# Kernel tuning notes

Hardware: AMD Instinct MI355X
Metric: run time of the kernel (lower is better)

Reference implementation:

```python
import jax, jax.numpy as jnp
import numpy as np

L, D, H, DH, S, B, V = 8, 1024, 16, 64, 1024, 4, 32000
EPS = 1e-5


def layernorm(x, s, b):
    m = x.mean(-1, keepdims=True)
    v = ((x - m) ** 2).mean(-1, keepdims=True)
    return (x - m) * jax.lax.rsqrt(v + EPS) * s + b


def setup_inputs() -> dict:
    key = jax.random.key(0)
    ks = jax.random.split(key, 12)
    sd = 0.02
    inp = {
        'idx': jax.random.randint(ks[0], (B, S), 0, V),
        'tok_emb': jax.random.normal(ks[1], (V, D), jnp.float32) * sd,
        'pos_emb': jax.random.normal(ks[2], (S, D), jnp.float32) * sd,
        'ln1_s': jnp.ones((L, D), jnp.float32),
        'ln1_b': jnp.zeros((L, D), jnp.float32),
        'wq': jax.random.normal(ks[3], (L, H, D, DH), jnp.float32) * sd,
        'wk': jax.random.normal(ks[4], (L, H, D, DH), jnp.float32) * sd,
        'wv': jax.random.normal(ks[5], (L, H, D, DH), jnp.float32) * sd,
        'wproj': jax.random.normal(ks[6], (L, D, D), jnp.float32) * sd,  # stored [D_in, D_out]
        'ln2_s': jnp.ones((L, D), jnp.float32),
        'ln2_b': jnp.zeros((L, D), jnp.float32),
        'w1': jax.random.normal(ks[7], (L, D, 4 * D), jnp.float32) * sd,
        'b1': jnp.zeros((L, 4 * D), jnp.float32),
        'w2': jax.random.normal(ks[8], (L, 4 * D, D), jnp.float32) * sd,
        'b2': jnp.zeros((L, D), jnp.float32),
        'lnf_s': jnp.ones((D,), jnp.float32),
        'lnf_b': jnp.zeros((D,), jnp.float32),
        'lm_w': jax.random.normal(ks[9], (D, V), jnp.float32) * sd,  # stored [D_in, V]
        'lm_b': jnp.zeros((V,), jnp.float32),
    }
    return inp


def reference(idx, tok_emb, pos_emb, ln1_s, ln1_b, wq, wk, wv, wproj,
              ln2_s, ln2_b, w1, b1, w2, b2, lnf_s, lnf_b, lm_w, lm_b):
    T = idx.shape[1]
    x = tok_emb[idx] + pos_emb[:T]  # [B,T,D]
    mask = jnp.tril(jnp.ones((T, T), bool))
    scale = DH ** -0.5
    for l in range(L):  # fixed small layer count
        h = layernorm(x, ln1_s[l], ln1_b[l])
        q = jnp.einsum('bsd,hde->bhse', h, wq[l])
        k = jnp.einsum('bsd,hde->bhse', h, wk[l])
        v = jnp.einsum('bsd,hde->bhse', h, wv[l])
        att = jnp.einsum('bhse,bhte->bhst', q, k) * scale
        att = jnp.where(mask, att, -jnp.inf)
        att = jax.nn.softmax(att, axis=-1)  # dropout=0.0 -> identity
        o = jnp.einsum('bhst,bhte->bhse', att, v)
        o = o.transpose(0, 2, 1, 3).reshape(x.shape)  # concat heads: [B,T,H*DH]
        x = x + o @ wproj[l]
        h2 = layernorm(x, ln2_s[l], ln2_b[l])
        x = x + jax.nn.relu(h2 @ w1[l] + b1[l]) @ w2[l] + b2[l]
    x = layernorm(x, lnf_s, lnf_b)
    logits = x @ lm_w + lm_b  # [B,T,V]
    return logits
```

## Files before the change

kernel.cpp:

```cpp
#include <hip/hip_runtime.h>
#include <hip/hip_bf16.h>

#define LL 8
#define DD 1024
#define HH 16
#define DHH 64
#define SS 1024
#define BB 4
#define VV 32000
#define MM (BB * SS)

typedef unsigned short u16;
typedef __attribute__((ext_vector_type(8))) short short8v;
typedef __attribute__((ext_vector_type(4))) float f32x4;
typedef unsigned int __attribute__((address_space(1))) guint;
typedef unsigned int __attribute__((address_space(3))) luint;

__device__ __forceinline__ float bf2f_lo(unsigned u) { return __uint_as_float(u << 16); }
__device__ __forceinline__ u16 f2bf(float f) {
  unsigned x = __float_as_uint(f);
  return (u16)((x + 0x7fffu + ((x >> 16) & 1u)) >> 16);
}

__global__ __launch_bounds__(256) void embed_kernel(
    const int* __restrict__ idx, const float* __restrict__ tok,
    const float* __restrict__ pos, float* __restrict__ x) {
  int i = blockIdx.x * blockDim.x + threadIdx.x;
  int elem = i * 4;
  int row = elem / DD;
  int d = elem % DD;
  int s = row % SS;
  int t = idx[row];
  float4 tv = *(const float4*)(tok + (size_t)t * DD + d);
  float4 pv = *(const float4*)(pos + (size_t)s * DD + d);
  tv.x += pv.x; tv.y += pv.y; tv.z += pv.z; tv.w += pv.w;
  *(float4*)(x + (size_t)elem) = tv;
}

__global__ __launch_bounds__(256) void ln_bf16_kernel(
    const float* __restrict__ x, const float* __restrict__ sc,
    const float* __restrict__ bi, u16* __restrict__ out) {
  const int row = blockIdx.x;
  const int tid = threadIdx.x;
  __shared__ float red[4];
  float4 v = ((const float4*)(x + (size_t)row * DD))[tid];
  float s = v.x + v.y + v.z + v.w;
  #pragma unroll
  for (int off = 32; off; off >>= 1) s += __shfl_down(s, off);
  if ((tid & 63) == 0) red[tid >> 6] = s;
  __syncthreads();
  float mean = (red[0] + red[1] + red[2] + red[3]) * (1.f / DD);
  float dx = v.x - mean, dy = v.y - mean, dz = v.z - mean, dw = v.w - mean;
  float vs = dx * dx + dy * dy + dz * dz + dw * dw;
  __syncthreads();
  #pragma unroll
  for (int off = 32; off; off >>= 1) vs += __shfl_down(vs, off);
  if ((tid & 63) == 0) red[tid >> 6] = vs;
  __syncthreads();
  float var = (red[0] + red[1] + red[2] + red[3]) * (1.f / DD);
  float rstd = rsqrtf(var + 1e-5f);
  float4 s4 = ((const float4*)sc)[tid];
  float4 b4 = ((const float4*)bi)[tid];
  ushort4 o;
  o.x = f2bf(dx * rstd * s4.x + b4.x);
  o.y = f2bf(dy * rstd * s4.y + b4.y);
  o.z = f2bf(dz * rstd * s4.z + b4.z);
  o.w = f2bf(dw * rstd * s4.w + b4.w);
  *(ushort4*)(out + (size_t)row * DD + tid * 4) = o;
}

template <bool HEADW>
__global__ __launch_bounds__(256) void convT_kernel(
    const float* __restrict__ W, u16* __restrict__ BT, int K, int N,
    size_t lstride) {
  __shared__ float tile[32][33];
  const int n0 = blockIdx.x * 32, k0 = blockIdx.y * 32, l = blockIdx.z;
  const int tx = threadIdx.x & 31, ty = threadIdx.x >> 5;
  const float* Wl;
  int ld;
  if (HEADW) {
    const int h = n0 >> 6;
    Wl = W + ((size_t)(l * HH + h) * K) * 64 + (n0 & 63);
    ld = 64;
  } else {
    Wl = W + (size_t)l * K * N + n0;
    ld = N;
  }
  #pragma unroll
  for (int i = 0; i < 4; ++i)
    tile[ty + 8 * i][tx] = Wl[(size_t)(k0 + ty + 8 * i) * ld + tx];
  __syncthreads();
  u16* out = BT + (size_t)l * lstride;
  #pragma unroll
  for (int i = 0; i < 4; ++i)
    out[(size_t)(n0 + ty + 8 * i) * K + k0 + tx] = f2bf(tile[tx][ty + 8 * i]);
}

__global__ __launch_bounds__(256) void transpose_v(
    const u16* __restrict__ qkv, u16* __restrict__ vt) {
  __shared__ u16 t[32][33];
  const int s0 = blockIdx.x * 32, d0 = blockIdx.y * 32;
  const int tx = threadIdx.x & 31, ty = threadIdx.x >> 5;
  #pragma unroll
  for (int i = 0; i < 4; ++i)
    t[ty + 8 * i][tx] = qkv[(size_t)(s0 + ty + 8 * i) * 3072 + 2048 + d0 + tx];
  __syncthreads();
  #pragma unroll
  for (int i = 0; i < 4; ++i)
    vt[(size_t)(d0 + ty + 8 * i) * MM + s0 + tx] = t[tx][ty + 8 * i];
}

#define BARRIER __builtin_amdgcn_s_barrier()
#define MEMFENCE asm volatile("" ::: "memory")

#define LDA_(BUF, KH, F) \
  (*(const short8v*)&As[BUF][KH][(wm * 128 + (F) * 16 + (lane & 15)) * 32 + rg])
#define LDB_(BUF, KH, NF) \
  (*(const short8v*)&Bs[BUF][KH][(wn * 64 + (NF) * 16 + (lane & 15)) * 32 + rg])
#define LDS_A(S0,S1,S2,S3, BUF, KH, FB) { \
  S0 = LDA_(BUF, KH, (FB) + 0); S1 = LDA_(BUF, KH, (FB) + 1); \
  S2 = LDA_(BUF, KH, (FB) + 2); S3 = LDA_(BUF, KH, (FB) + 3); }
#define LDS_B(S0,S1,S2,S3, BUF, KH) { \
  S0 = LDB_(BUF, KH, 0); S1 = LDB_(BUF, KH, 1); \
  S2 = LDB_(BUF, KH, 2); S3 = LDB_(BUF, KH, 3); }
#define STAGE_A(BUF, KH, KT) do { \
  __builtin_amdgcn_global_load_lds((const guint*)(Abase + (KT) * 64 + (KH) * 32), \
      (luint*)(&As[BUF][KH][tid * 8]), 16, 0, 0); \
  __builtin_amdgcn_global_load_lds((const guint*)(Abase + (size_t)128 * K + (KT) * 64 + (KH) * 32), \
      (luint*)(&As[BUF][KH][(tid + 512) * 8]), 16, 0, 0); \
} while (0)
#define STAGE_B(BUF, KH, KT) do { \
  __builtin_amdgcn_global_load_lds((const guint*)(Bbase + (KT) * 64 + (KH) * 32), \
      (luint*)(&Bs[BUF][KH][tid * 8]), 16, 0, 0); \
  __builtin_amdgcn_global_load_lds((const guint*)(Bbase + (size_t)128 * K + (KT) * 64 + (KH) * 32), \
      (luint*)(&Bs[BUF][KH][(tid + 512) * 8]), 16, 0, 0); \
} while (0)
#define MROW(F, AQ, B0,B1,B2,B3) \
  acc[F][0] = __builtin_amdgcn_mfma_f32_16x16x32_bf16(AQ, B0, acc[F][0], 0, 0, 0); \
  acc[F][1] = __builtin_amdgcn_mfma_f32_16x16x32_bf16(AQ, B1, acc[F][1], 0, 0, 0); \
  acc[F][2] = __builtin_amdgcn_mfma_f32_16x16x32_bf16(AQ, B2, acc[F][2], 0, 0, 0); \
  acc[F][3] = __builtin_amdgcn_mfma_f32_16x16x32_bf16(AQ, B3, acc[F][3], 0, 0, 0);
#define MFMA16S(FB, A0,A1,A2,A3, B0,B1,B2,B3) \
  MROW((FB) + 0, A0, B0,B1,B2,B3) MROW((FB) + 1, A1, B0,B1,B2,B3) \
  MROW((FB) + 2, A2, B0,B1,B2,B3) MROW((FB) + 3, A3, B0,B1,B2,B3)

#define TILE4(CUR, KT, ST1, ST2, V1STR, V3STR, LD4, LGK4STR) { \
  const int cur_ = (CUR); \
   \
  MEMFENCE; \
  LDS_A(aN0,aN1,aN2,aN3, cur_, 0, 4); \
  if (ST1) { STAGE_A(cur_ ^ 1, 1, (KT) + 1); } \
  asm volatile("s_waitcnt " V1STR ::: "memory"); \
  asm volatile("s_waitcnt lgkmcnt(4)" ::: "memory"); \
  BARRIER; \
  __builtin_amdgcn_s_setprio(1); \
  MFMA16S(0, aP0,aP1,aP2,aP3, bP0,bP1,bP2,bP3); \
  __builtin_amdgcn_s_setprio(0); \
   \
  MEMFENCE; \
  LDS_A(aP0,aP1,aP2,aP3, cur_, 1, 0); \
  LDS_B(bN0,bN1,bN2,bN3, cur_, 1); \
  if (ST1) { STAGE_B(cur_ ^ 1, 1, (KT) + 1); } \
  asm volatile("s_waitcnt lgkmcnt(8)" ::: "memory"); \
  BARRIER; \
  __builtin_amdgcn_s_setprio(1); \
  MFMA16S(4, aN0,aN1,aN2,aN3, bP0,bP1,bP2,bP3); \
  __builtin_amdgcn_s_setprio(0); \
   \
  MEMFENCE; \
  LDS_A(aN0,aN1,aN2,aN3, cur_, 1, 4); \
  if (ST2) { STAGE_A(cur_, 0, (KT) + 2); } \
  asm volatile("s_waitcnt " V3STR ::: "memory"); \
  asm volatile("s_waitcnt lgkmcnt(4)" ::: "memory"); \
  BARRIER; \
  __builtin_amdgcn_s_setprio(1); \
  MFMA16S(0, aP0,aP1,aP2,aP3, bN0,bN1,bN2,bN3); \
  __builtin_amdgcn_s_setprio(0); \
   \
  MEMFENCE; \
  if (LD4) { LDS_A(aP0,aP1,aP2,aP3, cur_ ^ 1, 0, 0); \
             LDS_B(bP0,bP1,bP2,bP3, cur_ ^ 1, 0); } \
  if (ST2) { STAGE_B(cur_, 0, (KT) + 2); } \
  asm volatile("s_waitcnt " LGK4STR ::: "memory"); \
  BARRIER; \
  __builtin_amdgcn_s_setprio(1); \
  MFMA16S(4, aN0,aN1,aN2,aN3, bN0,bN1,bN2,bN3); \
  __builtin_amdgcn_s_setprio(0); \
}

template <bool BIAS, bool RELU, bool RESID, bool OBF16>
__global__ __launch_bounds__(512, 2) void gemm8(
    const u16* __restrict__ A, const u16* __restrict__ BT,
    const float* __restrict__ bias, const float* __restrict__ resid,
    void* __restrict__ Cv, int M, int N, int K) {
  __shared__ u16 As[2][2][8192];
  __shared__ u16 Bs[2][2][8192];
  const int tid = threadIdx.x;
  const int lane = tid & 63, wave = tid >> 6;
  const int wm = wave >> 2, wn = wave & 3;
  const int nwg = gridDim.x;
  const int bid = blockIdx.x;
  const int wg = ((nwg & 7) == 0) ? ((bid & 7) * (nwg >> 3) + (bid >> 3)) : bid;
  const int nmt = M >> 8;
  const int m0 = (wg % nmt) * 256;
  const int n0 = (wg / nmt) * 256;
  const int NT = K >> 6;
  const int sr = tid >> 2;
  const int ssc = (((tid & 3) ^ ((tid >> 3) & 3)) * 8);
  const u16* Abase = A + (size_t)(m0 + sr) * K + ssc;
  const u16* Bbase = BT + (size_t)(n0 + sr) * K + ssc;
  const int rg = (((lane >> 4) ^ ((lane >> 1) & 3)) * 8);

  f32x4 acc[8][4] = {};
  short8v aP0, aP1, aP2, aP3, aN0, aN1, aN2, aN3;
  short8v bP0, bP1, bP2, bP3, bN0, bN1, bN2, bN3;

  STAGE_A(0, 0, 0); STAGE_B(0, 0, 0);
  STAGE_A(0, 1, 0); STAGE_B(0, 1, 0);
  STAGE_A(1, 0, 1); STAGE_B(1, 0, 1);
  asm volatile("s_waitcnt vmcnt(8)" ::: "memory");
  BARRIER;
  MEMFENCE;
  LDS_A(aP0,aP1,aP2,aP3, 0, 0, 0);
  LDS_B(bP0,bP1,bP2,bP3, 0, 0);

  int kt = 0;
  for (; kt < NT - 2; ++kt) {
    TILE4(kt & 1, kt, true, true, "vmcnt(6)", "vmcnt(6)", true, "lgkmcnt(8)");
  }
  TILE4(kt & 1, kt, true, false, "vmcnt(6)", "vmcnt(4)", true, "lgkmcnt(8)");
  ++kt;
  TILE4(kt & 1, kt, false, false, "vmcnt(0)", "vmcnt(0)", false, "lgkmcnt(0)");

  #pragma unroll
  for (int f = 0; f < 8; ++f) {
    #pragma unroll
    for (int n = 0; n < 4; ++n) {
      const int col = n0 + wn * 64 + n * 16 + (lane & 15);
      #pragma unroll
      for (int r = 0; r < 4; ++r) {
        const int row = m0 + wm * 128 + f * 16 + (lane >> 4) * 4 + r;
        float v = acc[f][n][r];
        if (BIAS) v += bias[col];
        if (RELU) v = fmaxf(v, 0.f);
        if (RESID) v += resid[(size_t)row * N + col];
        if (OBF16)
          ((u16*)Cv)[(size_t)row * N + col] = f2bf(v);
        else
          ((float*)Cv)[(size_t)row * N + col] = v;
      }
    }
  }
}

#define LDA4_(BUF, KH, F) \
  (*(const short8v*)&As[BUF][KH][(wm * 64 + (F) * 16 + (lane & 15)) * 32 + rg])
#define LDB4_(BUF, KH, NF) \
  (*(const short8v*)&Bs[BUF][KH][(wn * 64 + (NF) * 16 + (lane & 15)) * 32 + rg])
#define STAGE_A4(BUF, KH, KT) do { \
  __builtin_amdgcn_global_load_lds((const guint*)(Abase + (KT) * 64 + (KH) * 32), \
      (luint*)(&As[BUF][KH][tid * 8]), 16, 0, 0); \
  __builtin_amdgcn_global_load_lds((const guint*)(Abase + (size_t)64 * K + (KT) * 64 + (KH) * 32), \
      (luint*)(&As[BUF][KH][(tid + 256) * 8]), 16, 0, 0); \
} while (0)
#define STAGE_B4(BUF, KH, KT) do { \
  __builtin_amdgcn_global_load_lds((const guint*)(Bbase + (KT) * 64 + (KH) * 32), \
      (luint*)(&Bs[BUF][KH][tid * 8]), 16, 0, 0); \
  __builtin_amdgcn_global_load_lds((const guint*)(Bbase + (size_t)64 * K + (KT) * 64 + (KH) * 32), \
      (luint*)(&Bs[BUF][KH][(tid + 256) * 8]), 16, 0, 0); \
} while (0)
#define MFMA8S(F0, F1, A0, A1, B0,B1,B2,B3) \
  MROW(F0, A0, B0,B1,B2,B3) MROW(F1, A1, B0,B1,B2,B3)

#define TILE4P(CUR, KT, ST1, ST2, V1STR, V3STR, LD4, LGK4STR) { \
  const int cur_ = (CUR); \
   \
  MEMFENCE; \
  aN0 = LDA4_(cur_, 0, 2); aN1 = LDA4_(cur_, 0, 3); \
  if (ST1) { STAGE_A4(cur_ ^ 1, 1, (KT) + 1); } \
  asm volatile("s_waitcnt " V1STR ::: "memory"); \
  asm volatile("s_waitcnt lgkmcnt(2)" ::: "memory"); \
  BARRIER; \
  __builtin_amdgcn_s_setprio(1); \
  MFMA8S(0, 1, aP0, aP1, bP0,bP1,bP2,bP3); \
  __builtin_amdgcn_s_setprio(0); \
   \
  MEMFENCE; \
  aP0 = LDA4_(cur_, 1, 0); aP1 = LDA4_(cur_, 1, 1); \
  bN0 = LDB4_(cur_, 1, 0); bN1 = LDB4_(cur_, 1, 1); \
  bN2 = LDB4_(cur_, 1, 2); bN3 = LDB4_(cur_, 1, 3); \
  if (ST1) { STAGE_B4(cur_ ^ 1, 1, (KT) + 1); } \
  asm volatile("s_waitcnt lgkmcnt(6)" ::: "memory"); \
  BARRIER; \
  __builtin_amdgcn_s_setprio(1); \
  MFMA8S(2, 3, aN0, aN1, bP0,bP1,bP2,bP3); \
  __builtin_amdgcn_s_setprio(0); \
   \
  MEMFENCE; \
  aN0 = LDA4_(cur_, 1, 2); aN1 = LDA4_(cur_, 1, 3); \
  if (ST2) { STAGE_A4(cur_, 0, (KT) + 2); } \
  asm volatile("s_waitcnt " V3STR ::: "memory"); \
  asm volatile("s_waitcnt lgkmcnt(2)" ::: "memory"); \
  BARRIER; \
  __builtin_amdgcn_s_setprio(1); \
  MFMA8S(0, 1, aP0, aP1, bN0,bN1,bN2,bN3); \
  __builtin_amdgcn_s_setprio(0); \
   \
  MEMFENCE; \
  if (LD4) { aP0 = LDA4_(cur_ ^ 1, 0, 0); aP1 = LDA4_(cur_ ^ 1, 0, 1); \
             bP0 = LDB4_(cur_ ^ 1, 0, 0); bP1 = LDB4_(cur_ ^ 1, 0, 1); \
             bP2 = LDB4_(cur_ ^ 1, 0, 2); bP3 = LDB4_(cur_ ^ 1, 0, 3); } \
  if (ST2) { STAGE_B4(cur_, 0, (KT) + 2); } \
  asm volatile("s_waitcnt " LGK4STR ::: "memory"); \
  BARRIER; \
  __builtin_amdgcn_s_setprio(1); \
  MFMA8S(2, 3, aN0, aN1, bN0,bN1,bN2,bN3); \
  __builtin_amdgcn_s_setprio(0); \
}

template <bool BIAS, bool RELU, bool RESID, bool OBF16>
__global__ __launch_bounds__(256, 2) void gemm4p(
    const u16* __restrict__ A, const u16* __restrict__ BT,
    const float* __restrict__ bias, const float* __restrict__ resid,
    void* __restrict__ Cv, int M, int N, int K) {
  __shared__ u16 As[2][2][4096];
  __shared__ u16 Bs[2][2][4096];
  const int tid = threadIdx.x;
  const int lane = tid & 63, wave = tid >> 6;
  const int wm = wave >> 1, wn = wave & 1;
  const int m0 = blockIdx.x * 128, n0 = blockIdx.y * 128;
  const int NT = K >> 6;
  const int sr = tid >> 2;
  const int ssc = (((tid & 3) ^ ((tid >> 3) & 3)) * 8);
  const u16* Abase = A + (size_t)(m0 + sr) * K + ssc;
  const u16* Bbase = BT + (size_t)(n0 + sr) * K + ssc;
  const int rg = (((lane >> 4) ^ ((lane >> 1) & 3)) * 8);

  f32x4 acc[4][4] = {};
  short8v aP0, aP1, aN0, aN1;
  short8v bP0, bP1, bP2, bP3, bN0, bN1, bN2, bN3;

  STAGE_A4(0, 0, 0); STAGE_B4(0, 0, 0);
  STAGE_A4(0, 1, 0); STAGE_B4(0, 1, 0);
  STAGE_A4(1, 0, 1); STAGE_B4(1, 0, 1);
  asm volatile("s_waitcnt vmcnt(8)" ::: "memory");
  BARRIER;
  MEMFENCE;
  aP0 = LDA4_(0, 0, 0); aP1 = LDA4_(0, 0, 1);
  bP0 = LDB4_(0, 0, 0); bP1 = LDB4_(0, 0, 1);
  bP2 = LDB4_(0, 0, 2); bP3 = LDB4_(0, 0, 3);

  int kt = 0;
  for (; kt < NT - 2; ++kt) {
    TILE4P(kt & 1, kt, true, true, "vmcnt(6)", "vmcnt(6)", true, "lgkmcnt(6)");
  }
  TILE4P(kt & 1, kt, true, false, "vmcnt(6)", "vmcnt(4)", true, "lgkmcnt(6)");
  ++kt;
  TILE4P(kt & 1, kt, false, false, "vmcnt(0)", "vmcnt(0)", false, "lgkmcnt(0)");

  #pragma unroll
  for (int f = 0; f < 4; ++f) {
    #pragma unroll
    for (int n = 0; n < 4; ++n) {
      const int col = n0 + wn * 64 + n * 16 + (lane & 15);
      #pragma unroll
      for (int r = 0; r < 4; ++r) {
        const int row = m0 + wm * 64 + f * 16 + (lane >> 4) * 4 + r;
        float v = acc[f][n][r];
        if (BIAS) v += bias[col];
        if (RELU) v = fmaxf(v, 0.f);
        if (RESID) v += resid[(size_t)row * N + col];
        if (OBF16)
          ((u16*)Cv)[(size_t)row * N + col] = f2bf(v);
        else
          ((float*)Cv)[(size_t)row * N + col] = v;
      }
    }
  }
}

__global__ __launch_bounds__(256) void gemm_fb(
    const u16* __restrict__ A, const float* __restrict__ B,
    const float* __restrict__ bias, float* __restrict__ C, int M, int N, int K) {
  __shared__ alignas(16) float Asm[16][68];
  __shared__ alignas(16) float Bsm[16][68];
  const int tid = threadIdx.x;
  const int tx = tid & 15, ty = tid >> 4;
  const int m0 = blockIdx.y * 64, n0 = blockIdx.x * 64;
  const int ar = tid >> 2, ac = (tid & 3) * 4;
  const int br = tid >> 4, bc = (tid & 15) * 4;
  float acc[4][4] = {};
  for (int k0 = 0; k0 < K; k0 += 16) {
    ushort4 au = *(const ushort4*)(A + (size_t)(m0 + ar) * K + k0 + ac);
    float4 bv = *(const float4*)(B + (size_t)(k0 + br) * N + n0 + bc);
    Asm[ac + 0][ar] = bf2f_lo(au.x);
    Asm[ac + 1][ar] = bf2f_lo(au.y);
    Asm[ac + 2][ar] = bf2f_lo(au.z);
    Asm[ac + 3][ar] = bf2f_lo(au.w);
    *(float4*)&Bsm[br][bc] = bv;
    __syncthreads();
    #pragma unroll
    for (int kk = 0; kk < 16; ++kk) {
      float4 a = *(const float4*)&Asm[kk][ty * 4];
      float4 b = *(const float4*)&Bsm[kk][tx * 4];
      acc[0][0] += a.x * b.x; acc[0][1] += a.x * b.y; acc[0][2] += a.x * b.z; acc[0][3] += a.x * b.w;
      acc[1][0] += a.y * b.x; acc[1][1] += a.y * b.y; acc[1][2] += a.y * b.z; acc[1][3] += a.y * b.w;
      acc[2][0] += a.z * b.x; acc[2][1] += a.z * b.y; acc[2][2] += a.z * b.z; acc[2][3] += a.z * b.w;
      acc[3][0] += a.w * b.x; acc[3][1] += a.w * b.y; acc[3][2] += a.w * b.z; acc[3][3] += a.w * b.w;
    }
    __syncthreads();
  }
  #pragma unroll
  for (int i = 0; i < 4; ++i) {
    const int m = m0 + ty * 4 + i;
    #pragma unroll
    for (int j = 0; j < 4; ++j) {
      const int n = n0 + tx * 4 + j;
      C[(size_t)m * N + n] = acc[i][j] + bias[n];
    }
  }
}

__global__ __launch_bounds__(256) void attn_mfma(
    const u16* __restrict__ qkv, const u16* __restrict__ vt,
    u16* __restrict__ o) {
  __shared__ alignas(16) u16 Ksh[64 * 64];
  __shared__ alignas(16) u16 Vsh[64 * 64];
  __shared__ unsigned Plds[4][16 * 41];
  __shared__ float bcast[4][16];
  const int tid = threadIdx.x;
  const int lane = tid & 63, wave = tid >> 6;
  const int g = lane >> 4, qi = lane & 15;
  const int qt = blockIdx.x, h = blockIdx.y, b = blockIdx.z;
  const int q0w = qt * 64 + wave * 16;
  const int qloc = wave * 16 + qi;

  short8v qf0, qf1;
  {
    const u16* qp = qkv + ((size_t)b * SS + q0w + qi) * 3072 + h * DHH + g * 8;
    qf0 = *(const short8v*)qp;
    qf1 = *(const short8v*)(qp + 32);
  }

  f32x4 oacc[4] = {};
  float mrow = -1e30f, lrow = 0.f;

  for (int kt = 0; kt <= qt; ++kt) {
    __syncthreads();
    #pragma unroll
    for (int u = 0; u < 2; ++u) {
      const int unit = tid + 256 * u;
      const int row = unit >> 3, ch = unit & 7;
      const int sch = ch ^ (row & 7);
      __builtin_amdgcn_global_load_lds(
          (const guint*)(qkv + ((size_t)b * SS + kt * 64 + row) * 3072 + 1024 + h * DHH + sch * 8),
          (luint*)(Ksh + unit * 8), 16, 0, 0);
      __builtin_amdgcn_global_load_lds(
          (const guint*)(vt + ((size_t)(h * DHH + row)) * MM + b * SS + kt * 64 + sch * 8),
          (luint*)(Vsh + unit * 8), 16, 0, 0);
    }
    __syncthreads();

    f32x4 st[4] = {};
    #pragma unroll
    for (int t = 0; t < 4; ++t) {
      const int row = t * 16 + qi;
      const int swz = (row & 7) << 4;
      short8v kf0 = *(const short8v*)(Ksh + row * 64 + (((g * 16) ^ swz) >> 1));
      short8v kf1 = *(const short8v*)(Ksh + row * 64 + (((64 + g * 16) ^ swz) >> 1));
      st[t] = __builtin_amdgcn_mfma_f32_16x16x32_bf16(kf0, qf0, st[t], 0, 0, 0);
      st[t] = __builtin_amdgcn_mfma_f32_16x16x32_bf16(kf1, qf1, st[t], 0, 0, 0);
    }

    if (kt == qt) {
      #pragma unroll
      for (int t = 0; t < 4; ++t)
        #pragma unroll
        for (int r = 0; r < 4; ++r)
          if (t * 16 + 4 * g + r > qloc) st[t][r] = -1e30f;
    }

    float mt = st[0][0];
    #pragma unroll
    for (int t = 0; t < 4; ++t)
      #pragma unroll
      for (int r = 0; r < 4; ++r) mt = fmaxf(mt, st[t][r]);
    mt = fmaxf(mt, __shfl_xor(mt, 16));
    mt = fmaxf(mt, __shfl_xor(mt, 32));
    const float mnew = fmaxf(mrow, mt * 0.125f);
    const float corr = __expf(mrow - mnew);
    float pl = 0.f;
    #pragma unroll
    for (int t = 0; t < 4; ++t) {
      #pragma unroll
      for (int r2 = 0; r2 < 2; ++r2) {
        float plo = __expf(fmaf(st[t][2 * r2], 0.125f, -mnew));
        float phi = __expf(fmaf(st[t][2 * r2 + 1], 0.125f, -mnew));
        pl += plo + phi;
        Plds[wave][qi * 41 + 8 * t + 2 * g + r2] =
            (unsigned)f2bf(plo) | ((unsigned)f2bf(phi) << 16);
      }
    }
    pl += __shfl_xor(pl, 16);
    pl += __shfl_xor(pl, 32);
    lrow = lrow * corr + pl;
    mrow = mnew;

    if (g == 0) bcast[wave][qi] = corr;
    float c0 = bcast[wave][g * 4 + 0];
    float c1 = bcast[wave][g * 4 + 1];
    float c2 = bcast[wave][g * 4 + 2];
    float c3 = bcast[wave][g * 4 + 3];
    #pragma unroll
    for (int dvt = 0; dvt < 4; ++dvt) {
      oacc[dvt][0] *= c0; oacc[dvt][1] *= c1;
      oacc[dvt][2] *= c2; oacc[dvt][3] *= c3;
    }

    union U8 { unsigned u[4]; short8v s8; };
    U8 pa0, pa1;
    #pragma unroll
    for (int c = 0; c < 4; ++c) {
      pa0.u[c] = Plds[wave][qi * 41 + g * 4 + c];
      pa1.u[c] = Plds[wave][qi * 41 + 16 + g * 4 + c];
    }
    #pragma unroll
    for (int dvt = 0; dvt < 4; ++dvt) {
      const int row = dvt * 16 + qi;
      const int swz = (row & 7) << 4;
      short8v v0 = *(const short8v*)(Vsh + row * 64 + (((g * 16) ^ swz) >> 1));
      short8v v1 = *(const short8v*)(Vsh + row * 64 + (((64 + g * 16) ^ swz) >> 1));
      oacc[dvt] = __builtin_amdgcn_mfma_f32_16x16x32_bf16(pa0.s8, v0, oacc[dvt], 0, 0, 0);
      oacc[dvt] = __builtin_amdgcn_mfma_f32_16x16x32_bf16(pa1.s8, v1, oacc[dvt], 0, 0, 0);
    }
  }

  if (g == 0) bcast[wave][qi] = 1.f / lrow;
  float i0 = bcast[wave][g * 4 + 0];
  float i1 = bcast[wave][g * 4 + 1];
  float i2 = bcast[wave][g * 4 + 2];
  float i3 = bcast[wave][g * 4 + 3];
  #pragma unroll
  for (int dvt = 0; dvt < 4; ++dvt) {
    const int col = h * DHH + dvt * 16 + qi;
    o[((size_t)b * SS + q0w + g * 4 + 0) * DD + col] = f2bf(oacc[dvt][0] * i0);
    o[((size_t)b * SS + q0w + g * 4 + 1) * DD + col] = f2bf(oacc[dvt][1] * i1);
    o[((size_t)b * SS + q0w + g * 4 + 2) * DD + col] = f2bf(oacc[dvt][2] * i2);
    o[((size_t)b * SS + q0w + g * 4 + 3) * DD + col] = f2bf(oacc[dvt][3] * i3);
  }
}

extern "C" void kernel_launch(void* const* d_in, const int* in_sizes, int n_in,
                              void* d_out, int out_size, void* d_ws, size_t ws_size,
                              hipStream_t stream) {
  const int* idx = (const int*)d_in[0];
  const float* tok_emb = (const float*)d_in[1];
  const float* pos_emb = (const float*)d_in[2];
  const float* ln1_s = (const float*)d_in[3];
  const float* ln1_b = (const float*)d_in[4];
  const float* wq = (const float*)d_in[5];
  const float* wk = (const float*)d_in[6];
  const float* wv = (const float*)d_in[7];
  const float* wproj = (const float*)d_in[8];
  const float* ln2_s = (const float*)d_in[9];
  const float* ln2_b = (const float*)d_in[10];
  const float* w1 = (const float*)d_in[11];
  const float* b1 = (const float*)d_in[12];
  const float* w2 = (const float*)d_in[13];
  const float* b2 = (const float*)d_in[14];
  const float* lnf_s = (const float*)d_in[15];
  const float* lnf_b = (const float*)d_in[16];
  const float* lm_w = (const float*)d_in[17];
  const float* lm_b = (const float*)d_in[18];

  const size_t MD = (size_t)MM * DD;

  u16* sc0 = (u16*)d_out;
  u16* BTqkv = sc0;
  u16* BTp = BTqkv + (size_t)LL * 3072 * DD;
  u16* BTw1 = BTp + (size_t)LL * DD * DD;
  u16* BTw2 = BTw1 + (size_t)LL * DD * 4 * DD;
  u16* qkvb = BTw2 + (size_t)LL * DD * 4 * DD;
  u16* vtb = qkvb + (size_t)MM * 3072;
  u16* ob = vtb + MD;
  u16* tmp = ob + MD;

  float* x = (float*)d_ws;
  u16* h = (u16*)((char*)d_ws + MD * 4);
  u16* BTlm = (u16*)((char*)d_ws + MD * 4 + MD * 2);
  const bool big_ws = ws_size >= (MD * 4 + MD * 2 + (size_t)VV * DD * 2);

  const dim3 blk(256);

  convT_kernel<true><<<dim3(DD / 32, DD / 32, LL), blk, 0, stream>>>(
      wq, BTqkv, DD, DD, (size_t)3072 * DD);
  convT_kernel<true><<<dim3(DD / 32, DD / 32, LL), blk, 0, stream>>>(
      wk, BTqkv + (size_t)DD * DD, DD, DD, (size_t)3072 * DD);
  convT_kernel<true><<<dim3(DD / 32, DD / 32, LL), blk, 0, stream>>>(
      wv, BTqkv + (size_t)2 * DD * DD, DD, DD, (size_t)3072 * DD);
  convT_kernel<false><<<dim3(DD / 32, DD / 32, LL), blk, 0, stream>>>(
      wproj, BTp, DD, DD, (size_t)DD * DD);
  convT_kernel<false><<<dim3(4 * DD / 32, DD / 32, LL), blk, 0, stream>>>(
      w1, BTw1, DD, 4 * DD, (size_t)DD * 4 * DD);
  convT_kernel<false><<<dim3(DD / 32, 4 * DD / 32, LL), blk, 0, stream>>>(
      w2, BTw2, 4 * DD, DD, (size_t)4 * DD * DD);
  if (big_ws)
    convT_kernel<false><<<dim3(VV / 32, DD / 32, 1), blk, 0, stream>>>(
        lm_w, BTlm, DD, VV, (size_t)VV * DD);

  embed_kernel<<<(MM * DD / 4 + 255) / 256, blk, 0, stream>>>(idx, tok_emb, pos_emb, x);

  for (int l = 0; l < LL; ++l) {
    ln_bf16_kernel<<<MM, blk, 0, stream>>>(x, ln1_s + l * DD, ln1_b + l * DD, h);
    gemm8<false, false, false, true><<<dim3((MM / 256) * (3072 / 256)), dim3(512), 0, stream>>>(
        h, BTqkv + (size_t)l * 3072 * DD, nullptr, nullptr, qkvb, MM, 3072, DD);
    transpose_v<<<dim3(MM / 32, DD / 32), blk, 0, stream>>>(qkvb, vtb);
    attn_mfma<<<dim3(SS / 64, HH, BB), blk, 0, stream>>>(qkvb, vtb, ob);
    gemm4p<false, false, true, false><<<dim3(MM / 128, DD / 128), blk, 0, stream>>>(
        ob, BTp + (size_t)l * DD * DD, nullptr, x, x, MM, DD, DD);
    ln_bf16_kernel<<<MM, blk, 0, stream>>>(x, ln2_s + l * DD, ln2_b + l * DD, h);
    gemm8<true, true, false, true><<<dim3((MM / 256) * (4 * DD / 256)), dim3(512), 0, stream>>>(
        h, BTw1 + (size_t)l * DD * 4 * DD, b1 + (size_t)l * 4 * DD, nullptr, tmp,
        MM, 4 * DD, DD);
    gemm4p<true, false, true, false><<<dim3(MM / 128, DD / 128), blk, 0, stream>>>(
        tmp, BTw2 + (size_t)l * 4 * DD * DD, b2 + (size_t)l * DD, x, x, MM, DD, 4 * DD);
  }

  ln_bf16_kernel<<<MM, blk, 0, stream>>>(x, lnf_s, lnf_b, h);
  if (big_ws) {
    gemm8<true, false, false, false><<<dim3((MM / 256) * (VV / 256)), dim3(512), 0, stream>>>(
        h, BTlm, lm_b, nullptr, (float*)d_out, MM, VV, DD);
  } else {
    gemm_fb<<<dim3(VV / 64, MM / 64), blk, 0, stream>>>(
        h, lm_w, lm_b, (float*)d_out, MM, VV, DD);
  }
}
```

Measured before the change: 2.429 ms.

## Enlarge attention query tile to 128 rows with 8 waves and reverse block order

The attention kernel now runs 512 threads (8 waves) per block, covering 128 query rows instead of 64. Each K/V tile loaded into shared memory is therefore reused by twice as many waves, halving global K/V traffic per query. Block indices are reversed so the longest causal blocks are scheduled first for better load balance. Waves whose queries lie entirely before the current key tile skip compute but still join the barriers, which leaves some MFMA work idle and halves the grid size.

Measured after the change: 2.392 ms. No clear change (-1.5%).

```diff
diff --git a/kernel.cpp b/kernel.cpp
--- a/kernel.cpp
+++ b/kernel.cpp
@@ -112,6 +112,11 @@
 
 #define BARRIER __builtin_amdgcn_s_barrier()
 #define MEMFENCE asm volatile("" ::: "memory")
+#define MROW(F, AQ, B0,B1,B2,B3) \
+  acc[F][0] = __builtin_amdgcn_mfma_f32_16x16x32_bf16(AQ, B0, acc[F][0], 0, 0, 0); \
+  acc[F][1] = __builtin_amdgcn_mfma_f32_16x16x32_bf16(AQ, B1, acc[F][1], 0, 0, 0); \
+  acc[F][2] = __builtin_amdgcn_mfma_f32_16x16x32_bf16(AQ, B2, acc[F][2], 0, 0, 0); \
+  acc[F][3] = __builtin_amdgcn_mfma_f32_16x16x32_bf16(AQ, B3, acc[F][3], 0, 0, 0);
 
 #define LDA_(BUF, KH, F) \
   (*(const short8v*)&As[BUF][KH][(wm * 128 + (F) * 16 + (lane & 15)) * 32 + rg])
@@ -135,11 +140,6 @@
   __builtin_amdgcn_global_load_lds((const guint*)(Bbase + (size_t)128 * K + (KT) * 64 + (KH) * 32), \
       (luint*)(&Bs[BUF][KH][(tid + 512) * 8]), 16, 0, 0); \
 } while (0)
-#define MROW(F, AQ, B0,B1,B2,B3) \
-  acc[F][0] = __builtin_amdgcn_mfma_f32_16x16x32_bf16(AQ, B0, acc[F][0], 0, 0, 0); \
-  acc[F][1] = __builtin_amdgcn_mfma_f32_16x16x32_bf16(AQ, B1, acc[F][1], 0, 0, 0); \
-  acc[F][2] = __builtin_amdgcn_mfma_f32_16x16x32_bf16(AQ, B2, acc[F][2], 0, 0, 0); \
-  acc[F][3] = __builtin_amdgcn_mfma_f32_16x16x32_bf16(AQ, B3, acc[F][3], 0, 0, 0);
 #define MFMA16S(FB, A0,A1,A2,A3, B0,B1,B2,B3) \
   MROW((FB) + 0, A0, B0,B1,B2,B3) MROW((FB) + 1, A1, B0,B1,B2,B3) \
   MROW((FB) + 2, A2, B0,B1,B2,B3) MROW((FB) + 3, A3, B0,B1,B2,B3)
@@ -274,7 +274,6 @@
 
 #define TILE4P(CUR, KT, ST1, ST2, V1STR, V3STR, LD4, LGK4STR) { \
   const int cur_ = (CUR); \
-   \
   MEMFENCE; \
   aN0 = LDA4_(cur_, 0, 2); aN1 = LDA4_(cur_, 0, 3); \
   if (ST1) { STAGE_A4(cur_ ^ 1, 1, (KT) + 1); } \
@@ -284,7 +283,6 @@
   __builtin_amdgcn_s_setprio(1); \
   MFMA8S(0, 1, aP0, aP1, bP0,bP1,bP2,bP3); \
   __builtin_amdgcn_s_setprio(0); \
-   \
   MEMFENCE; \
   aP0 = LDA4_(cur_, 1, 0); aP1 = LDA4_(cur_, 1, 1); \
   bN0 = LDB4_(cur_, 1, 0); bN1 = LDB4_(cur_, 1, 1); \
@@ -295,7 +293,6 @@
   __builtin_amdgcn_s_setprio(1); \
   MFMA8S(2, 3, aN0, aN1, bP0,bP1,bP2,bP3); \
   __builtin_amdgcn_s_setprio(0); \
-   \
   MEMFENCE; \
   aN0 = LDA4_(cur_, 1, 2); aN1 = LDA4_(cur_, 1, 3); \
   if (ST2) { STAGE_A4(cur_, 0, (KT) + 2); } \
@@ -305,7 +302,6 @@
   __builtin_amdgcn_s_setprio(1); \
   MFMA8S(0, 1, aP0, aP1, bN0,bN1,bN2,bN3); \
   __builtin_amdgcn_s_setprio(0); \
-   \
   MEMFENCE; \
   if (LD4) { aP0 = LDA4_(cur_ ^ 1, 0, 0); aP1 = LDA4_(cur_ ^ 1, 0, 1); \
              bP0 = LDB4_(cur_ ^ 1, 0, 0); bP1 = LDB4_(cur_ ^ 1, 0, 1); \
@@ -421,19 +417,20 @@
   }
 }
 
-__global__ __launch_bounds__(256) void attn_mfma(
+__global__ __launch_bounds__(512) void attn_mfma(
     const u16* __restrict__ qkv, const u16* __restrict__ vt,
     u16* __restrict__ o) {
   __shared__ alignas(16) u16 Ksh[64 * 64];
   __shared__ alignas(16) u16 Vsh[64 * 64];
-  __shared__ unsigned Plds[4][16 * 41];
-  __shared__ float bcast[4][16];
+  __shared__ unsigned Plds[8][16 * 41];
+  __shared__ float bcast[8][16];
   const int tid = threadIdx.x;
   const int lane = tid & 63, wave = tid >> 6;
   const int g = lane >> 4, qi = lane & 15;
-  const int qt = blockIdx.x, h = blockIdx.y, b = blockIdx.z;
-  const int q0w = qt * 64 + wave * 16;
-  const int qloc = wave * 16 + qi;
+  const int qt = (SS / 128 - 1) - blockIdx.x;
+  const int h = blockIdx.y, b = blockIdx.z;
+  const int q0w = qt * 128 + wave * 16;
+  const int ktmax = 2 * qt + 1;
 
   short8v qf0, qf1;
   {
@@ -445,93 +442,95 @@
   f32x4 oacc[4] = {};
   float mrow = -1e30f, lrow = 0.f;
 
-  for (int kt = 0; kt <= qt; ++kt) {
+  for (int kt = 0; kt <= ktmax; ++kt) {
     __syncthreads();
-    #pragma unroll
-    for (int u = 0; u < 2; ++u) {
-      const int unit = tid + 256 * u;
-      const int row = unit >> 3, ch = unit & 7;
+    {
+      const int row = tid >> 3, ch = tid & 7;
       const int sch = ch ^ (row & 7);
       __builtin_amdgcn_global_load_lds(
           (const guint*)(qkv + ((size_t)b * SS + kt * 64 + row) * 3072 + 1024 + h * DHH + sch * 8),
-          (luint*)(Ksh + unit * 8), 16, 0, 0);
+          (luint*)(Ksh + tid * 8), 16, 0, 0);
       __builtin_amdgcn_global_load_lds(
           (const guint*)(vt + ((size_t)(h * DHH + row)) * MM + b * SS + kt * 64 + sch * 8),
-          (luint*)(Vsh + unit * 8), 16, 0, 0);
+          (luint*)(Vsh + tid * 8), 16, 0, 0);
     }
     __syncthreads();
 
-    f32x4 st[4] = {};
-    #pragma unroll
-    for (int t = 0; t < 4; ++t) {
-      const int row = t * 16 + qi;
-      const int swz = (row & 7) << 4;
-      short8v kf0 = *(const short8v*)(Ksh + row * 64 + (((g * 16) ^ swz) >> 1));
-      short8v kf1 = *(const short8v*)(Ksh + row * 64 + (((64 + g * 16) ^ swz) >> 1));
-      st[t] = __builtin_amdgcn_mfma_f32_16x16x32_bf16(kf0, qf0, st[t], 0, 0, 0);
-      st[t] = __builtin_amdgcn_mfma_f32_16x16x32_bf16(kf1, qf1, st[t], 0, 0, 0);
-    }
-
-    if (kt == qt) {
+    const bool active = (kt * 64 <= q0w + 15);
+    if (active) {
+      f32x4 st[4] = {};
+      #pragma unroll
+      for (int t = 0; t < 4; ++t) {
+        const int row = t * 16 + qi;
+        const int swz = (row & 7) << 4;
+        short8v kf0 = *(const short8v*)(Ksh + row * 64 + (((g * 16) ^ swz) >> 1));
+        short8v kf1 = *(const short8v*)(Ksh + row * 64 + (((64 + g * 16) ^ swz) >> 1));
+        st[t] = __builtin_amdgcn_mfma_f32_16x16x32_bf16(kf0, qf0, st[t], 0, 0, 0);
+        st[t] = __builtin_amdgcn_mfma_f32_16x16x32_bf16(kf1, qf1, st[t], 0, 0, 0);
+      }
+
+      const int diag = q0w + qi - kt * 64;
+      if (diag < 63) {
+        #pragma unroll
+        for (int t = 0; t < 4; ++t)
+          #pragma unroll
+          for (int r = 0; r < 4; ++r)
+            if (t * 16 + 4 * g + r > diag) st[t][r] = -1e30f;
+      }
+
+      float mt = st[0][0];
       #pragma unroll
       for (int t = 0; t < 4; ++t)
         #pragma unroll
-        for (int r = 0; r < 4; ++r)
-          if (t * 16 + 4 * g + r > qloc) st[t][r] = -1e30f;
-    }
-
-    float mt = st[0][0];
-    #pragma unroll
-    for (int t = 0; t < 4; ++t)
-      #pragma unroll
-      for (int r = 0; r < 4; ++r) mt = fmaxf(mt, st[t][r]);
-    mt = fmaxf(mt, __shfl_xor(mt, 16));
-    mt = fmaxf(mt, __shfl_xor(mt, 32));
-    const float mnew = fmaxf(mrow, mt * 0.125f);
-    const float corr = __expf(mrow - mnew);
-    float pl = 0.f;
-    #pragma unroll
-    for (int t = 0; t < 4; ++t) {
-      #pragma unroll
-      for (int r2 = 0; r2 < 2; ++r2) {
-        float plo = __expf(fmaf(st[t][2 * r2], 0.125f, -mnew));
-        float phi = __expf(fmaf(st[t][2 * r2 + 1], 0.125f, -mnew));
-        pl += plo + phi;
-        Plds[wave][qi * 41 + 8 * t + 2 * g + r2] =
-            (unsigned)f2bf(plo) | ((unsigned)f2bf(phi) << 16);
-      }
-    }
-    pl += __shfl_xor(pl, 16);
-    pl += __shfl_xor(pl, 32);
-    lrow = lrow * corr + pl;
-    mrow = mnew;
-
-    if (g == 0) bcast[wave][qi] = corr;
-    float c0 = bcast[wave][g * 4 + 0];
-    float c1 = bcast[wave][g * 4 + 1];
-    float c2 = bcast[wave][g * 4 + 2];
-    float c3 = bcast[wave][g * 4 + 3];
-    #pragma unroll
-    for (int dvt = 0; dvt < 4; ++dvt) {
-      oacc[dvt][0] *= c0; oacc[dvt][1] *= c1;
-      oacc[dvt][2] *= c2; oacc[dvt][3] *= c3;
-    }
-
-    union U8 { unsigned u[4]; short8v s8; };
-    U8 pa0, pa1;
-    #pragma unroll
-    for (int c = 0; c < 4; ++c) {
-      pa0.u[c] = Plds[wave][qi * 41 + g * 4 + c];
-      pa1.u[c] = Plds[wave][qi * 41 + 16 + g * 4 + c];
-    }
-    #pragma unroll
-    for (int dvt = 0; dvt < 4; ++dvt) {
-      const int row = dvt * 16 + qi;
-      const int swz = (row & 7) << 4;
-      short8v v0 = *(const short8v*)(Vsh + row * 64 + (((g * 16) ^ swz) >> 1));
-      short8v v1 = *(const short8v*)(Vsh + row * 64 + (((64 + g * 16) ^ swz) >> 1));
-      oacc[dvt] = __builtin_amdgcn_mfma_f32_16x16x32_bf16(pa0.s8, v0, oacc[dvt], 0, 0, 0);
-      oacc[dvt] = __builtin_amdgcn_mfma_f32_16x16x32_bf16(pa1.s8, v1, oacc[dvt], 0, 0, 0);
+        for (int r = 0; r < 4; ++r) mt = fmaxf(mt, st[t][r]);
+      mt = fmaxf(mt, __shfl_xor(mt, 16));
+      mt = fmaxf(mt, __shfl_xor(mt, 32));
+      const float mnew = fmaxf(mrow, mt * 0.125f);
+      const float corr = __expf(mrow - mnew);
+      float pl = 0.f;
+      #pragma unroll
+      for (int t = 0; t < 4; ++t) {
+        #pragma unroll
+        for (int r2 = 0; r2 < 2; ++r2) {
+          float plo = __expf(fmaf(st[t][2 * r2], 0.125f, -mnew));
+          float phi = __expf(fmaf(st[t][2 * r2 + 1], 0.125f, -mnew));
+          pl += plo + phi;
+          Plds[wave][qi * 41 + 8 * t + 2 * g + r2] =
+              (unsigned)f2bf(plo) | ((unsigned)f2bf(phi) << 16);
+        }
+      }
+      pl += __shfl_xor(pl, 16);
+      pl += __shfl_xor(pl, 32);
+      lrow = lrow * corr + pl;
+      mrow = mnew;
+
+      if (g == 0) bcast[wave][qi] = corr;
+      float c0 = bcast[wave][g * 4 + 0];
+      float c1 = bcast[wave][g * 4 + 1];
+      float c2 = bcast[wave][g * 4 + 2];
+      float c3 = bcast[wave][g * 4 + 3];
+      #pragma unroll
+      for (int dvt = 0; dvt < 4; ++dvt) {
+        oacc[dvt][0] *= c0; oacc[dvt][1] *= c1;
+        oacc[dvt][2] *= c2; oacc[dvt][3] *= c3;
+      }
+
+      union U8 { unsigned u[4]; short8v s8; };
+      U8 pa0, pa1;
+      #pragma unroll
+      for (int c = 0; c < 4; ++c) {
+        pa0.u[c] = Plds[wave][qi * 41 + g * 4 + c];
+        pa1.u[c] = Plds[wave][qi * 41 + 16 + g * 4 + c];
+      }
+      #pragma unroll
+      for (int dvt = 0; dvt < 4; ++dvt) {
+        const int row = dvt * 16 + qi;
+        const int swz = (row & 7) << 4;
+        short8v v0 = *(const short8v*)(Vsh + row * 64 + (((g * 16) ^ swz) >> 1));
+        short8v v1 = *(const short8v*)(Vsh + row * 64 + (((64 + g * 16) ^ swz) >> 1));
+        oacc[dvt] = __builtin_amdgcn_mfma_f32_16x16x32_bf16(pa0.s8, v0, oacc[dvt], 0, 0, 0);
+        oacc[dvt] = __builtin_amdgcn_mfma_f32_16x16x32_bf16(pa1.s8, v1, oacc[dvt], 0, 0, 0);
+      }
     }
   }
 
@@ -615,7 +614,7 @@
     gemm8<false, false, false, true><<<dim3((MM / 256) * (3072 / 256)), dim3(512), 0, stream>>>(
         h, BTqkv + (size_t)l * 3072 * DD, nullptr, nullptr, qkvb, MM, 3072, DD);
     transpose_v<<<dim3(MM / 32, DD / 32), blk, 0, stream>>>(qkvb, vtb);
-    attn_mfma<<<dim3(SS / 64, HH, BB), blk, 0, stream>>>(qkvb, vtb, ob);
+    attn_mfma<<<dim3(SS / 128, HH, BB), dim3(512), 0, stream>>>(qkvb, vtb, ob);
     gemm4p<false, false, true, false><<<dim3(MM / 128, DD / 128), blk, 0, stream>>>(
         ob, BTp + (size_t)l * DD * DD, nullptr, x, x, MM, DD, DD);
     ln_bf16_kernel<<<MM, blk, 0, stream>>>(x, ln2_s + l * DD, ln2_b + l * DD, h);
```
